# Optimization experiments

Hardware: AMD Instinct MI355X
Metric: run time of the kernel (lower is better)

The kernel has to match this reference:

```python
import jax, jax.numpy as jnp
import numpy as np

N, B, T, S, E, R = 4, 8, 512, 512, 1024, 1024


def setup_inputs() -> dict:
    key = jax.random.key(0)
    k1, k2, k3, k4, k5 = jax.random.split(key, 5)
    return {
        "query": jax.random.normal(k1, (1, B, T, E), dtype=jnp.float32),
        "key_value_states": jax.random.normal(k2, (N, B, S, R), dtype=jnp.float32),
        "attention_mask": jax.random.normal(k3, (1, B, T, S), dtype=jnp.float32),
        "Wk": jax.random.normal(k4, (E, R), dtype=jnp.float32) * (1.0 / np.sqrt(R)),
        "bk": jax.random.normal(k5, (E,), dtype=jnp.float32) * 0.01,
    }


def reference(query, key_value_states, attention_mask, Wk, bk):
    # k_proj: [N,B,S,R] @ [R,E] + bias -> [N,B,S,E]
    key = jnp.einsum("nbsr,er->nbse", key_value_states, Wk) + bk
    # QK^T (no scaling), query broadcast over N: [N,B,T,S]
    scores = jnp.einsum("bte,nbse->nbts", query[0], key)
    scores = scores + attention_mask  # mask broadcast over N
    attn = jax.nn.softmax(scores, axis=-1)
    # weights @ raw key_value_states (NOT projected key): [N,B,T,R]
    out = jnp.einsum("nbts,nbsr->nbtr", attn, key_value_states)
    return out
```

## Files before the change

### kernel.cpp

```cpp
#include <hip/hip_runtime.h>

typedef unsigned short u16;
typedef unsigned int u32;
typedef unsigned long long u64;

typedef __bf16 bfrag __attribute__((ext_vector_type(8)));
typedef float f32x4 __attribute__((ext_vector_type(4)));

typedef __attribute__((address_space(1))) char* gas1_p;
typedef __attribute__((address_space(3))) char* las3_p;

#define DI __device__ __forceinline__

DI u16 f2bf(float f) {
  u32 u = __float_as_uint(f);
  u += 0x7FFFu + ((u >> 16) & 1u);
  return (u16)(u >> 16);
}
DI float bf2f(u16 h) { return __uint_as_float(((u32)h) << 16); }

DI void gload16(const void* g, void* l) {
  __builtin_amdgcn_global_load_lds((gas1_p)(u64)g, (las3_p)(u32)(u64)l, 16, 0, 0);
}

template <int WH, int WTH, int WTL>
__global__ __launch_bounds__(256) void k_trsplit64(const float* __restrict__ in,
                                                   u16* __restrict__ hi, u16* __restrict__ lo,
                                                   u16* __restrict__ thi, u16* __restrict__ tlo,
                                                   int rows, int cols) {
  __shared__ float tile[64][65];
  const u64 zoff = (u64)blockIdx.z * (u64)rows * (u64)cols;
  const int r0 = threadIdx.x >> 4;
  const int c4 = (threadIdx.x & 15) << 2;
  const float* src = in + zoff + (u64)(blockIdx.y * 64 + r0) * cols + blockIdx.x * 64 + c4;
#pragma unroll
  for (int p = 0; p < 4; ++p) {
    float4 v = *reinterpret_cast<const float4*>(src + (u64)(p * 16) * cols);
    tile[r0 + p * 16][c4 + 0] = v.x;
    tile[r0 + p * 16][c4 + 1] = v.y;
    tile[r0 + p * 16][c4 + 2] = v.z;
    tile[r0 + p * 16][c4 + 3] = v.w;
  }
  __syncthreads();
  if constexpr (WH) {
    const int rr = threadIdx.x >> 3;
    const int cc = (threadIdx.x & 7) << 3;
#pragma unroll
    for (int p = 0; p < 2; ++p) {
      const int r = rr + p * 32;
      u32 h[4], l[4];
#pragma unroll
      for (int j = 0; j < 4; ++j) {
        float a = tile[r][cc + 2 * j], b = tile[r][cc + 2 * j + 1];
        u16 ha = f2bf(a), hb = f2bf(b);
        h[j] = (u32)ha | ((u32)hb << 16);
        l[j] = (u32)f2bf(a - bf2f(ha)) | ((u32)f2bf(b - bf2f(hb)) << 16);
      }
      const u64 o = zoff + (u64)(blockIdx.y * 64 + r) * cols + blockIdx.x * 64 + cc;
      *reinterpret_cast<uint4*>(hi + o) = make_uint4(h[0], h[1], h[2], h[3]);
      *reinterpret_cast<uint4*>(lo + o) = make_uint4(l[0], l[1], l[2], l[3]);
    }
  }
  if constexpr (WTH) {
#pragma unroll
    for (int p = 0; p < 2; ++p) {
      const int id = threadIdx.x + p * 256;
      const int col = id >> 3;
      const int s8 = (id & 7) << 3;
      u32 h[4], l[4];
#pragma unroll
      for (int j = 0; j < 4; ++j) {
        float a = tile[s8 + 2 * j][col], b = tile[s8 + 2 * j + 1][col];
        u16 ha = f2bf(a), hb = f2bf(b);
        h[j] = (u32)ha | ((u32)hb << 16);
        if constexpr (WTL)
          l[j] = (u32)f2bf(a - bf2f(ha)) | ((u32)f2bf(b - bf2f(hb)) << 16);
      }
      const u64 o = zoff + (u64)(blockIdx.x * 64 + col) * rows + blockIdx.y * 64 + s8;
      *reinterpret_cast<uint4*>(thi + o) = make_uint4(h[0], h[1], h[2], h[3]);
      if constexpr (WTL)
        *reinterpret_cast<uint4*>(tlo + o) = make_uint4(l[0], l[1], l[2], l[3]);
    }
  }
}

template <int X3, int AF32, int BF32, int FM, int FN, int WR, int WC,
          int ADDMASK, int SPLITOUT>
__global__ __launch_bounds__(WR * WC * 64, 2) void k_gemmF(
    const void* Ap, const u16* Aploi, const void* Bp, const u16* Bploi,
    float* __restrict__ Cf, u16* __restrict__ Chi, u16* __restrict__ Clo,
    const float* __restrict__ Mask,
    int K, int N, int mt, int nt,
    u64 aStride, int aMask, u64 bStride, u64 cStride) {
  constexpr int NTHR = WR * WC * 64;
  constexpr int BM = WR * FM * 16, BN = WC * FN * 16;
  constexpr int ACH = AF32 ? ((BM * 9 + NTHR - 1) / NTHR) * NTHR : BM * 4;
  constexpr int BCH = BF32 ? ((BN * 9 + NTHR - 1) / NTHR) * NTHR : BN * 4;
  constexpr int A_SZ = AF32 ? ACH * 8 : BM * 32 * (1 + X3);
  constexpr int B_SZ = BF32 ? BCH * 8 : BN * 32 * (1 + X3);
  constexpr int AL0 = BM * 32;
  constexpr int BL0 = BN * 32;
  constexpr int TILE = A_SZ + B_SZ;
  constexpr int CA = ACH / NTHR, CB = BCH / NTHR;
  __shared__ u16 lds[2 * TILE];

  const int tid = threadIdx.x, lane = tid & 63;
  const int wid = tid >> 6, wr = wid / WC, wc = wid % WC;

  const int g = (blockIdx.x & 7) * (gridDim.x >> 3) + (blockIdx.x >> 3);
  const int z = g / (mt * nt);
  const int rem = g - z * (mt * nt);
  const int ty = rem / nt, tx = rem - ty * nt;

  const u64 aOff = (u64)(z & aMask) * aStride;
  const u64 bOff = (u64)z * bStride;
  const float* gAf = nullptr;
  const u16* gA = nullptr;
  const u16* gAl = nullptr;
  if constexpr (AF32) {
    gAf = (const float*)Ap + aOff + (u64)ty * (u32)BM * (u32)K;
  } else {
    gA = (const u16*)Ap + aOff + (u64)ty * (u32)BM * (u32)K;
    if constexpr (X3) gAl = Aploi + aOff + (u64)ty * (u32)BM * (u32)K;
  }
  const float* gBf = nullptr;
  const u16* gB = nullptr;
  const u16* gBl = nullptr;
  if constexpr (BF32) {
    gBf = (const float*)Bp + bOff + (u64)tx * (u32)BN * (u32)K;
  } else {
    gB = (const u16*)Bp + bOff + (u64)tx * (u32)BN * (u32)K;
    if constexpr (X3) gBl = Bploi + bOff + (u64)tx * (u32)BN * (u32)K;
  }

  u64 aG[CA]; u32 aLd[CA];
#pragma unroll
  for (int i = 0; i < CA; ++i) {
    const int c = i * NTHR + tid;
    if constexpr (AF32) {
      const int row = c / 9, cc = c - row * 9;
      aG[i] = (row < BM && cc < 8) ? ((u64)row * (u32)K + (u32)(cc * 4)) : 0;
      aLd[i] = c * 8;
    } else {
      const int row = c >> 2, ks = c & 3;
      aG[i] = (u64)row * (u32)K + (u32)((ks ^ ((row >> 1) & 3)) << 3);
      aLd[i] = c << 3;
    }
  }
  u64 bG[CB]; u32 bLd[CB];
#pragma unroll
  for (int i = 0; i < CB; ++i) {
    const int c = i * NTHR + tid;
    if constexpr (BF32) {
      const int row = c / 9, cc = c - row * 9;
      bG[i] = (row < BN && cc < 8) ? ((u64)row * (u32)K + (u32)(cc * 4)) : 0;
      bLd[i] = c * 8;
    } else {
      const int row = c >> 2, ks = c & 3;
      bG[i] = (u64)row * (u32)K + (u32)((ks ^ ((row >> 1) & 3)) << 3);
      bLd[i] = c << 3;
    }
  }

  f32x4 acc[FM][FN];
#pragma unroll
  for (int m = 0; m < FM; ++m)
#pragma unroll
    for (int n = 0; n < FN; ++n) acc[m][n] = (f32x4){0.f, 0.f, 0.f, 0.f};

  auto STAGE = [&](int bufU, int k0) {
#pragma unroll
    for (int i = 0; i < CA; ++i) {
      if constexpr (AF32) {
        gload16(gAf + aG[i] + (u32)k0, &lds[bufU + aLd[i]]);
      } else {
        gload16(gA + aG[i] + (u32)k0, &lds[bufU + aLd[i]]);
        if constexpr (X3) gload16(gAl + aG[i] + (u32)k0, &lds[bufU + AL0 + aLd[i]]);
      }
    }
#pragma unroll
    for (int i = 0; i < CB; ++i) {
      if constexpr (BF32) {
        gload16(gBf + bG[i] + (u32)k0, &lds[bufU + A_SZ + bLd[i]]);
      } else {
        gload16(gB + bG[i] + (u32)k0, &lds[bufU + A_SZ + bLd[i]]);
        if constexpr (X3) gload16(gBl + bG[i] + (u32)k0, &lds[bufU + A_SZ + BL0 + bLd[i]]);
      }
    }
  };

  const int swz = (((lane >> 1) & 3) ^ (lane >> 4)) << 3;
  auto COMPUTE = [&](int bufU) {
    bfrag ah[FM], al[FM], bh[FN], bl[FN];
#pragma unroll
    for (int m = 0; m < FM; ++m) {
      const int row = wr * (FM * 16) + m * 16 + (lane & 15);
      if constexpr (AF32) {
        const u32 base = bufU + (u32)row * 72 + (u32)(lane >> 4) * 16;
        f32x4 p0 = *reinterpret_cast<const f32x4*>(&lds[base]);
        f32x4 p1 = *reinterpret_cast<const f32x4*>(&lds[base + 8]);
#pragma unroll
        for (int j = 0; j < 8; ++j) {
          float f = j < 4 ? p0[j] : p1[j - 4];
          __bf16 h = (__bf16)f;
          ah[m][j] = h;
          al[m][j] = (__bf16)(f - (float)h);
        }
      } else {
        const int idx = bufU + row * 32 + swz;
        ah[m] = *reinterpret_cast<const bfrag*>(&lds[idx]);
        if constexpr (X3) al[m] = *reinterpret_cast<const bfrag*>(&lds[idx + AL0]);
      }
    }
#pragma unroll
    for (int n = 0; n < FN; ++n) {
      const int row = wc * (FN * 16) + n * 16 + (lane & 15);
      if constexpr (BF32) {
        const u32 base = bufU + A_SZ + (u32)row * 72 + (u32)(lane >> 4) * 16;
        f32x4 p0 = *reinterpret_cast<const f32x4*>(&lds[base]);
        f32x4 p1 = *reinterpret_cast<const f32x4*>(&lds[base + 8]);
#pragma unroll
        for (int j = 0; j < 8; ++j) {
          float f = j < 4 ? p0[j] : p1[j - 4];
          __bf16 h = (__bf16)f;
          bh[n][j] = h;
          bl[n][j] = (__bf16)(f - (float)h);
        }
      } else {
        const int idx = bufU + A_SZ + row * 32 + swz;
        bh[n] = *reinterpret_cast<const bfrag*>(&lds[idx]);
        if constexpr (X3) bl[n] = *reinterpret_cast<const bfrag*>(&lds[idx + BL0]);
      }
    }
#pragma unroll
    for (int m = 0; m < FM; ++m)
#pragma unroll
      for (int n = 0; n < FN; ++n) {
        acc[m][n] = __builtin_amdgcn_mfma_f32_16x16x32_bf16(ah[m], bh[n], acc[m][n], 0, 0, 0);
        if constexpr (X3) {
          acc[m][n] = __builtin_amdgcn_mfma_f32_16x16x32_bf16(ah[m], bl[n], acc[m][n], 0, 0, 0);
          acc[m][n] = __builtin_amdgcn_mfma_f32_16x16x32_bf16(al[m], bh[n], acc[m][n], 0, 0, 0);
        }
      }
  };

  const int NT = K >> 5;
  STAGE(0, 0);
  asm volatile("s_waitcnt vmcnt(0)" ::: "memory");
  __builtin_amdgcn_s_barrier();
  int buf = 0;
  for (int t = 0; t < NT; ++t) {
    if (t + 1 < NT) STAGE(TILE - buf, (t + 1) << 5);
    COMPUTE(buf);
    if (t + 1 < NT) {
      asm volatile("s_waitcnt vmcnt(0)" ::: "memory");
      __builtin_amdgcn_s_barrier();
      buf = TILE - buf;
    }
  }

  const u64 cOff = (u64)z * cStride;
  const u64 mOff = (u64)(z & aMask) * cStride;
  const int rB = ty * BM + wr * (FM * 16) + (lane >> 4) * 4;
  const int cB = tx * BN + wc * (FN * 16) + (lane & 15);
#pragma unroll
  for (int m = 0; m < FM; ++m)
#pragma unroll
    for (int n = 0; n < FN; ++n)
#pragma unroll
      for (int j = 0; j < 4; ++j) {
        const int rr = rB + m * 16 + j, cc = cB + n * 16;
        const u64 ci = cOff + (u64)rr * (u32)N + (u32)cc;
        float v = acc[m][n][j];
        if constexpr (ADDMASK) v += Mask[mOff + (u64)rr * (u32)N + (u32)cc];
        if constexpr (SPLITOUT) {
          u16 h = f2bf(v);
          Chi[ci] = h;
          Clo[ci] = f2bf(v - bf2f(h));
        } else {
          Cf[ci] = v;
        }
      }
}

__global__ __launch_bounds__(256) void k_softmax(const float* __restrict__ sc,
                                                 u16* __restrict__ attn) {
  const int row = blockIdx.x * 4 + (threadIdx.x >> 6);
  const int lane = threadIdx.x & 63;
  const float* srow = sc + (u64)row * 512 + lane * 8;
  float4 s0 = *reinterpret_cast<const float4*>(srow);
  float4 s1 = *reinterpret_cast<const float4*>(srow + 4);
  float x[8] = {s0.x, s0.y, s0.z, s0.w, s1.x, s1.y, s1.z, s1.w};
  float mx = x[0];
#pragma unroll
  for (int j = 1; j < 8; ++j) mx = fmaxf(mx, x[j]);
#pragma unroll
  for (int off = 32; off > 0; off >>= 1) mx = fmaxf(mx, __shfl_xor(mx, off));
  float sum = 0.f;
#pragma unroll
  for (int j = 0; j < 8; ++j) {
    x[j] = __expf(x[j] - mx);
    sum += x[j];
  }
#pragma unroll
  for (int off = 32; off > 0; off >>= 1) sum += __shfl_xor(sum, off);
  const float inv = 1.f / sum;
  u32 o[4];
#pragma unroll
  for (int j = 0; j < 4; ++j) {
    u16 e0 = f2bf(x[2 * j] * inv), e1 = f2bf(x[2 * j + 1] * inv);
    o[j] = (u32)e0 | ((u32)e1 << 16);
  }
  *reinterpret_cast<uint4*>(attn + (u64)row * 512 + lane * 8) = make_uint4(o[0], o[1], o[2], o[3]);
}

extern "C" void kernel_launch(void* const* d_in, const int* in_sizes, int n_in,
                              void* d_out, int out_size, void* d_ws, size_t ws_size,
                              hipStream_t stream) {
  const float* q = (const float*)d_in[0];
  const float* kvs = (const float*)d_in[1];
  const float* mask = (const float*)d_in[2];
  const float* Wk = (const float*)d_in[3];
  float* out = (float*)d_out;

  char* w = (char*)d_ws;
  u16* attn = (u16*)(w + 0);
  u16* wkt_hi = (u16*)(w + 16777216);
  u16* wkt_lo = (u16*)(w + 18874368);
  u16* qp_hi = (u16*)(w + 20971520);
  u16* qp_lo = (u16*)(w + 29360128);
  u16* kvt_hi = (u16*)(w + 104857600);
  float* sc = (float*)(w + 138412032);

  k_trsplit64<0, 1, 1><<<dim3(16, 16, 1), dim3(256), 0, stream>>>(
      Wk, (u16*)nullptr, (u16*)nullptr, wkt_hi, wkt_lo, 1024, 1024);
  k_trsplit64<0, 1, 0><<<dim3(16, 8, 32), dim3(256), 0, stream>>>(
      kvs, (u16*)nullptr, (u16*)nullptr, kvt_hi, (u16*)nullptr, 512, 1024);
  k_gemmF<1, 1, 0, 4, 4, 2, 2, 0, 1><<<dim3(256), dim3(256), 0, stream>>>(
      q, (const u16*)nullptr, wkt_hi, wkt_lo,
      (float*)nullptr, qp_hi, qp_lo, (const float*)nullptr,
      1024, 1024, 32, 8, (u64)0, 0, (u64)0, (u64)0);
  k_gemmF<1, 0, 1, 4, 4, 2, 2, 1, 0><<<dim3(512), dim3(256), 0, stream>>>(
      qp_hi, qp_lo, kvs, (const u16*)nullptr,
      sc, (u16*)nullptr, (u16*)nullptr, mask,
      1024, 512, 4, 4, (u64)524288, 7, (u64)524288, (u64)262144);
  k_softmax<<<dim3(4096), dim3(256), 0, stream>>>(sc, attn);
  k_gemmF<0, 0, 0, 8, 4, 2, 2, 0, 0><<<dim3(512), dim3(256), 0, stream>>>(
      attn, (const u16*)nullptr, kvt_hi, (const u16*)nullptr,
      out, (u16*)nullptr, (u16*)nullptr, (const float*)nullptr,
      512, 1024, 2, 8, (u64)262144, 31, (u64)524288, (u64)524288);

  (void)in_sizes; (void)n_in; (void)out_size; (void)ws_size;
}
```

Baseline: 159.5 us.

## Replace scores GEMM with 8-wave triple-buffered pipelined kernel with interleaved loads

Adds a dedicated 512-thread kernel for the Q·K^T scores GEMM (with mask add). It uses 256x128 tiles, a three-stage LDS ring fed by direct global-to-LDS loads, and swizzled A layout. Global loads are interleaved between MFMA phases, with explicit vmcnt waits and setprio. The fp32 B operand is split into bf16 hi/lo in registers, so the three-MFMA split-precision product is kept. The cost is heavy barrier usage and large LDS, which limits occupancy.

Result: slower. 171.9 us (+7.8%).

```diff
diff --git a/kernel.cpp b/kernel.cpp
--- a/kernel.cpp
+++ b/kernel.cpp
@@ -21,6 +21,14 @@
 
 DI void gload16(const void* g, void* l) {
   __builtin_amdgcn_global_load_lds((gas1_p)(u64)g, (las3_p)(u32)(u64)l, 16, 0, 0);
+}
+
+template <int N>
+DI void waitvm() {
+  if constexpr (N == 7)      asm volatile("s_waitcnt vmcnt(7)" ::: "memory");
+  else if constexpr (N == 6) asm volatile("s_waitcnt vmcnt(6)" ::: "memory");
+  else if constexpr (N == 4) asm volatile("s_waitcnt vmcnt(4)" ::: "memory");
+  else                       asm volatile("s_waitcnt vmcnt(0)" ::: "memory");
 }
 
 template <int WH, int WTH, int WTL>
@@ -283,6 +291,153 @@
       }
 }
 
+__global__ __launch_bounds__(512, 2) void k_s8(
+    const u16* __restrict__ Ah, const u16* __restrict__ Al,
+    const float* __restrict__ Bf, const float* __restrict__ Mask,
+    float* __restrict__ Cf) {
+  constexpr int ALO = 8192, B0 = 16384, TILE = 25600;
+  __shared__ u16 lds[3 * TILE];
+  const int tid = threadIdx.x, lane = tid & 63;
+  const int wid = tid >> 6, wr = wid >> 1, wc = wid & 1;
+
+  const int g = (blockIdx.x & 7) * 32 + (blockIdx.x >> 3);
+  const int z = g >> 3;
+  const int rem = g & 7;
+  const int ty = rem >> 2, tx = rem & 3;
+  const int b = z & 7;
+
+  const u16* gAh = Ah + (u64)b * 524288 + (u64)ty * 256 * 1024;
+  const u16* gAl = Al + (u64)b * 524288 + (u64)ty * 256 * 1024;
+  const float* gB = Bf + (u64)z * 524288 + (u64)tx * 128 * 1024;
+
+  u32 gOf[7]; u32 dOf[7];
+#pragma unroll
+  for (int i = 0; i < 7; ++i) {
+    const int c = (i < 6) ? i * 512 + tid : 3072 + (tid & 127);
+    if (c < 2048) {
+      const int c2 = c & 1023, row = c2 >> 2, ks = c2 & 3;
+      gOf[i] = (u32)row * 1024u + (u32)((ks ^ ((row >> 1) & 3)) << 3);
+      dOf[i] = (u32)((c < 1024 ? 0 : ALO) + c2 * 8);
+    } else {
+      const int cb = c - 2048, row = cb / 9, cc = cb - row * 9;
+      gOf[i] = (cc < 8) ? ((u32)row * 1024u + (u32)(cc * 4)) : 0u;
+      dOf[i] = (u32)(B0 + cb * 8);
+    }
+  }
+
+  f32x4 acc[4][4];
+#pragma unroll
+  for (int m = 0; m < 4; ++m)
+#pragma unroll
+    for (int n = 0; n < 4; ++n) acc[m][n] = (f32x4){0.f, 0.f, 0.f, 0.f};
+
+  const int swz = (((lane >> 1) & 3) ^ (lane >> 4)) << 3;
+  bfrag ah[2], al[2], bh[2], bl[2];
+
+  auto rdA = [&](int rb, int fm, int d) {
+    const int idx = rb + (wr * 64 + fm * 16 + (lane & 15)) * 32 + swz;
+    ah[d] = *reinterpret_cast<const bfrag*>(&lds[idx]);
+    al[d] = *reinterpret_cast<const bfrag*>(&lds[idx + ALO]);
+  };
+  auto rdB = [&](int rb, int fn, int d) {
+    const u32 base = (u32)rb + B0 + (u32)(wc * 64 + fn * 16 + (lane & 15)) * 72 +
+                     (u32)(lane >> 4) * 16;
+    f32x4 p0 = *reinterpret_cast<const f32x4*>(&lds[base]);
+    f32x4 p1 = *reinterpret_cast<const f32x4*>(&lds[base + 8]);
+#pragma unroll
+    for (int j = 0; j < 8; ++j) {
+      float f = j < 4 ? p0[j] : p1[j - 4];
+      __bf16 h = (__bf16)f;
+      bh[d][j] = h;
+      bl[d][j] = (__bf16)(f - (float)h);
+    }
+  };
+  auto MFMA12 = [&](int mp, int np) {
+#pragma unroll
+    for (int di = 0; di < 2; ++di)
+#pragma unroll
+      for (int dj = 0; dj < 2; ++dj) {
+        f32x4 a = acc[mp * 2 + di][np * 2 + dj];
+        a = __builtin_amdgcn_mfma_f32_16x16x32_bf16(ah[di], bh[dj], a, 0, 0, 0);
+        a = __builtin_amdgcn_mfma_f32_16x16x32_bf16(ah[di], bl[dj], a, 0, 0, 0);
+        a = __builtin_amdgcn_mfma_f32_16x16x32_bf16(al[di], bh[dj], a, 0, 0, 0);
+        acc[mp * 2 + di][np * 2 + dj] = a;
+      }
+  };
+
+#define STG(i, SRC, SB, K2) gload16(SRC + gOf[i] + (u32)(K2), &lds[(SB) + dOf[i]])
+
+#pragma unroll
+  for (int tt = 0; tt < 2; ++tt) {
+    const int sb = tt * TILE, k2 = tt * 32;
+    STG(0, gAh, sb, k2); STG(1, gAh, sb, k2);
+    STG(2, gAl, sb, k2); STG(3, gAl, sb, k2);
+    STG(4, gB, sb, k2);  STG(5, gB, sb, k2);  STG(6, gB, sb, k2);
+  }
+  waitvm<7>();
+  __builtin_amdgcn_s_barrier();
+
+  int bufIdx = 0;
+  for (int t = 0; t < 32; ++t) {
+    const int rb = bufIdx * TILE;
+    int sbIdx = bufIdx + 2; if (sbIdx >= 3) sbIdx -= 3;
+    const int sb = sbIdx * TILE;
+    const int k2 = (t + 2) << 5;
+    const bool st = (t + 2) < 32;
+
+    rdA(rb, 0, 0); rdA(rb, 1, 1);
+    rdB(rb, 0, 0); rdB(rb, 1, 1);
+    if (st) { STG(0, gAh, sb, k2); STG(1, gAh, sb, k2); }
+    __builtin_amdgcn_s_barrier();
+    __builtin_amdgcn_s_setprio(1);
+    MFMA12(0, 0);
+    __builtin_amdgcn_s_setprio(0);
+    __builtin_amdgcn_s_barrier();
+
+    rdB(rb, 2, 0); rdB(rb, 3, 1);
+    if (st) { STG(2, gAl, sb, k2); STG(3, gAl, sb, k2); }
+    __builtin_amdgcn_s_barrier();
+    __builtin_amdgcn_s_setprio(1);
+    MFMA12(0, 1);
+    __builtin_amdgcn_s_setprio(0);
+    __builtin_amdgcn_s_barrier();
+
+    rdA(rb, 2, 0); rdA(rb, 3, 1);
+    if (st) { STG(4, gB, sb, k2); STG(5, gB, sb, k2); }
+    __builtin_amdgcn_s_barrier();
+    __builtin_amdgcn_s_setprio(1);
+    MFMA12(1, 1);
+    __builtin_amdgcn_s_setprio(0);
+    __builtin_amdgcn_s_barrier();
+
+    rdB(rb, 0, 0); rdB(rb, 1, 1);
+    if (st) { STG(6, gB, sb, k2); }
+    __builtin_amdgcn_s_barrier();
+    __builtin_amdgcn_s_setprio(1);
+    MFMA12(1, 0);
+    __builtin_amdgcn_s_setprio(0);
+    if (st) waitvm<7>(); else waitvm<0>();
+    __builtin_amdgcn_s_barrier();
+
+    bufIdx = bufIdx + 1; if (bufIdx >= 3) bufIdx -= 3;
+  }
+#undef STG
+
+  const u64 cOff = (u64)z * 262144;
+  const int rB = ty * 256 + wr * 64 + (lane >> 4) * 4;
+  const int cB = tx * 128 + wc * 64 + (lane & 15);
+#pragma unroll
+  for (int m = 0; m < 4; ++m)
+#pragma unroll
+    for (int n = 0; n < 4; ++n)
+#pragma unroll
+      for (int j = 0; j < 4; ++j) {
+        const int rr = rB + m * 16 + j, cc = cB + n * 16;
+        float v = acc[m][n][j] + Mask[((u64)(b * 512 + rr)) * 512 + (u32)cc];
+        Cf[cOff + (u64)rr * 512 + (u32)cc] = v;
+      }
+}
+
 __global__ __launch_bounds__(256) void k_softmax(const float* __restrict__ sc,
                                                  u16* __restrict__ attn) {
   const int row = blockIdx.x * 4 + (threadIdx.x >> 6);
@@ -340,10 +495,7 @@
       q, (const u16*)nullptr, wkt_hi, wkt_lo,
       (float*)nullptr, qp_hi, qp_lo, (const float*)nullptr,
       1024, 1024, 32, 8, (u64)0, 0, (u64)0, (u64)0);
-  k_gemmF<1, 0, 1, 4, 4, 2, 2, 1, 0><<<dim3(512), dim3(256), 0, stream>>>(
-      qp_hi, qp_lo, kvs, (const u16*)nullptr,
-      sc, (u16*)nullptr, (u16*)nullptr, mask,
-      1024, 512, 4, 4, (u64)524288, 7, (u64)524288, (u64)262144);
+  k_s8<<<dim3(256), dim3(512), 0, stream>>>(qp_hi, qp_lo, kvs, mask, sc);
   k_softmax<<<dim3(4096), dim3(256), 0, stream>>>(sc, attn);
   k_gemmF<0, 0, 0, 8, 4, 2, 2, 0, 0><<<dim3(512), dim3(256), 0, stream>>>(
       attn, (const u16*)nullptr, kvt_hi, (const u16*)nullptr,
```

## Fuse key_value_states transpose into scores GEMM as side-write from LDS

Applied to the files above, without the earlier changes.

Removes the standalone transpose/bf16-convert kernel for key_value_states. The scores GEMM already stages kvs fp32 tiles into LDS, so some threads now read those tiles, convert them to bf16 and write the transposed layout needed by the final GEMM. This drops one launch and one full read of kvs. In exchange it adds LDS reads and global stores inside the GEMM main loop, which may slow that loop. It also relies on the grid covering each kvs tile exactly once across the tx/ty blocks.

Result: no change. 161.8 us (+1.4%).

```diff
diff --git a/kernel.cpp b/kernel.cpp
--- a/kernel.cpp
+++ b/kernel.cpp
@@ -85,11 +85,11 @@
 }
 
 template <int X3, int AF32, int BF32, int FM, int FN, int WR, int WC,
-          int ADDMASK, int SPLITOUT>
+          int ADDMASK, int SPLITOUT, int WRKVT>
 __global__ __launch_bounds__(WR * WC * 64, 2) void k_gemmF(
     const void* Ap, const u16* Aploi, const void* Bp, const u16* Bploi,
     float* __restrict__ Cf, u16* __restrict__ Chi, u16* __restrict__ Clo,
-    const float* __restrict__ Mask,
+    const float* __restrict__ Mask, u16* __restrict__ KvtOut,
     int K, int N, int mt, int nt,
     u64 aStride, int aMask, u64 bStride, u64 cStride) {
   constexpr int NTHR = WR * WC * 64;
@@ -244,6 +244,27 @@
       }
   };
 
+  auto SIDEWRITE = [&](int bufU, int k0) {
+    if (tid < 128) {
+      const int rl = (ty << 3) + (tid >> 4);
+      const int s8 = (tid & 15) << 3;
+      const int rot = tid & 7;
+      u32 pk[4];
+      u16 val[8];
+#pragma unroll
+      for (int j = 0; j < 8; ++j) {
+        const int je = (j + rot) & 7;
+        const float f = *reinterpret_cast<const float*>(
+            &lds[bufU + A_SZ + (u32)(s8 + je) * 72 + (u32)rl * 2]);
+        val[je] = f2bf(f);
+      }
+#pragma unroll
+      for (int j = 0; j < 4; ++j) pk[j] = (u32)val[2 * j] | ((u32)val[2 * j + 1] << 16);
+      const u64 o = (u64)z * ((u64)K * 512) + (u64)(k0 + rl) * 512 + (u32)(tx * BN + s8);
+      *reinterpret_cast<uint4*>(KvtOut + o) = make_uint4(pk[0], pk[1], pk[2], pk[3]);
+    }
+  };
+
   const int NT = K >> 5;
   STAGE(0, 0);
   asm volatile("s_waitcnt vmcnt(0)" ::: "memory");
@@ -251,6 +272,7 @@
   int buf = 0;
   for (int t = 0; t < NT; ++t) {
     if (t + 1 < NT) STAGE(TILE - buf, (t + 1) << 5);
+    if constexpr (WRKVT) SIDEWRITE(buf, t << 5);
     COMPUTE(buf);
     if (t + 1 < NT) {
       asm volatile("s_waitcnt vmcnt(0)" ::: "memory");
@@ -334,20 +356,18 @@
 
   k_trsplit64<0, 1, 1><<<dim3(16, 16, 1), dim3(256), 0, stream>>>(
       Wk, (u16*)nullptr, (u16*)nullptr, wkt_hi, wkt_lo, 1024, 1024);
-  k_trsplit64<0, 1, 0><<<dim3(16, 8, 32), dim3(256), 0, stream>>>(
-      kvs, (u16*)nullptr, (u16*)nullptr, kvt_hi, (u16*)nullptr, 512, 1024);
-  k_gemmF<1, 1, 0, 4, 4, 2, 2, 0, 1><<<dim3(256), dim3(256), 0, stream>>>(
+  k_gemmF<1, 1, 0, 4, 4, 2, 2, 0, 1, 0><<<dim3(256), dim3(256), 0, stream>>>(
       q, (const u16*)nullptr, wkt_hi, wkt_lo,
-      (float*)nullptr, qp_hi, qp_lo, (const float*)nullptr,
+      (float*)nullptr, qp_hi, qp_lo, (const float*)nullptr, (u16*)nullptr,
       1024, 1024, 32, 8, (u64)0, 0, (u64)0, (u64)0);
-  k_gemmF<1, 0, 1, 4, 4, 2, 2, 1, 0><<<dim3(512), dim3(256), 0, stream>>>(
+  k_gemmF<1, 0, 1, 4, 4, 2, 2, 1, 0, 1><<<dim3(512), dim3(256), 0, stream>>>(
       qp_hi, qp_lo, kvs, (const u16*)nullptr,
-      sc, (u16*)nullptr, (u16*)nullptr, mask,
+      sc, (u16*)nullptr, (u16*)nullptr, mask, kvt_hi,
       1024, 512, 4, 4, (u64)524288, 7, (u64)524288, (u64)262144);
   k_softmax<<<dim3(4096), dim3(256), 0, stream>>>(sc, attn);
-  k_gemmF<0, 0, 0, 8, 4, 2, 2, 0, 0><<<dim3(512), dim3(256), 0, stream>>>(
+  k_gemmF<0, 0, 0, 8, 4, 2, 2, 0, 0, 0><<<dim3(512), dim3(256), 0, stream>>>(
       attn, (const u16*)nullptr, kvt_hi, (const u16*)nullptr,
-      out, (u16*)nullptr, (u16*)nullptr, (const float*)nullptr,
+      out, (u16*)nullptr, (u16*)nullptr, (const float*)nullptr, (u16*)nullptr,
       512, 1024, 2, 8, (u64)262144, 31, (u64)524288, (u64)524288);
 
   (void)in_sizes; (void)n_in; (void)out_size; (void)ws_size;
```
